# Kernel tuning notes

Measured on AMD Instinct MI355X. Metric: run time of the kernel, lower is better.

## Reference

```python
import jax, jax.numpy as jnp
import numpy as np

N_HEAD = 16

def _rope(t, cos, sin):
    # t: [B,T,H,hd]; cos/sin: [T, hd//2]
    B, T, H, hd = t.shape
    tr = t.reshape(B, T, H, hd // 2, 2)
    t0, t1 = tr[..., 0], tr[..., 1]
    c = cos[None, :T, None, :]
    s = sin[None, :T, None, :]
    out = jnp.stack([t0 * c - t1 * s, t0 * s + t1 * c], axis=-1)
    return out.reshape(B, T, H, hd)

def setup_inputs() -> dict:
    key = jax.random.key(0)
    B, T, D = 2, 2048, 1024
    hd = D // N_HEAD
    ks = jax.random.split(key, 5)
    x = jax.random.normal(ks[0], (B, T, D), dtype=jnp.float32)
    Wq = jax.random.normal(ks[1], (D, D), dtype=jnp.float32) * 0.02
    Wk = jax.random.normal(ks[2], (D, D), dtype=jnp.float32) * 0.02
    Wv = jax.random.normal(ks[3], (D, D), dtype=jnp.float32) * 0.02
    Wo = jax.random.normal(ks[4], (D, D), dtype=jnp.float32) * 0.02
    # Real rotary tables (cos/sin of theta-based angles), matching precompute_freqs_cis
    theta = 10000.0
    inv_freq = 1.0 / (theta ** (np.arange(0, hd, 2, dtype=np.float32) / hd))
    ang = np.outer(np.arange(T, dtype=np.float32), inv_freq)  # [T, hd//2]
    freqs_cos = jnp.asarray(np.cos(ang), dtype=jnp.float32)
    freqs_sin = jnp.asarray(np.sin(ang), dtype=jnp.float32)
    return {"x": x, "Wq": Wq, "Wk": Wk, "Wv": Wv, "Wo": Wo,
            "freqs_cos": freqs_cos, "freqs_sin": freqs_sin}

def reference(x, Wq, Wk, Wv, Wo, freqs_cos, freqs_sin):
    B, T, D = x.shape
    H = N_HEAD
    hd = D // H
    scale = hd ** -0.5
    q = (x @ Wq.T).reshape(B, T, H, hd)
    k = (x @ Wk.T).reshape(B, T, H, hd)
    v = (x @ Wv.T).reshape(B, T, H, hd)
    q = _rope(q, freqs_cos, freqs_sin)
    k = _rope(k, freqs_cos, freqs_sin)
    # scores: [B,H,T,T]
    scores = jnp.einsum('bqhd,bkhd->bhqk', q, k) * scale
    causal = jnp.tril(jnp.ones((T, T), dtype=bool))
    scores = jnp.where(causal[None, None], scores, -jnp.inf)
    attn = jax.nn.softmax(scores, axis=-1)
    out = jnp.einsum('bhqk,bkhd->bqhd', attn, v).reshape(B, T, D)
    return out @ Wo.T
```

## Files before the change

### kernel.cpp

```cpp
#include <hip/hip_runtime.h>
#include <math.h>

typedef __bf16 bf16;
typedef __bf16 bf16x8 __attribute__((ext_vector_type(8)));
typedef __bf16 bf16x4 __attribute__((ext_vector_type(4)));
typedef __bf16 bf16x2 __attribute__((ext_vector_type(2)));
typedef float  f32x4  __attribute__((ext_vector_type(4)));

#define B_DIM 2
#define T_LEN 2048
#define D_DIM 1024
#define N_HEAD 16
#define HEAD_D 64
#define M_ROWS (B_DIM * T_LEN)

#define GLDS16(g, l)                                                          \
    __builtin_amdgcn_global_load_lds(                                         \
        (const __attribute__((address_space(1))) void*)(g),                   \
        (__attribute__((address_space(3))) void*)(l), 16, 0, 0)

__global__ void prep_cvt(const float* __restrict__ x, const float* __restrict__ wq,
                         const float* __restrict__ wk, const float* __restrict__ wv,
                         const float* __restrict__ wo, bf16* __restrict__ xb,
                         bf16* __restrict__ wqkv, bf16* __restrict__ wob) {
    int id = blockIdx.x * blockDim.x + threadIdx.x;
    if (id >= (1 << 21)) return;
    const float* src; bf16* dst; int off;
    if (id < (1 << 20)) { src = x; dst = xb; off = id; }
    else {
        int r = id - (1 << 20);
        int wi = r >> 18;
        off = r & ((1 << 18) - 1);
        src = wi == 0 ? wq : wi == 1 ? wk : wi == 2 ? wv : wo;
        dst = wi < 3 ? wqkv + ((size_t)wi << 20) : wob;
    }
    float4 v = reinterpret_cast<const float4*>(src)[off];
    bf16x4 w;
    w[0] = (bf16)v.x; w[1] = (bf16)v.y; w[2] = (bf16)v.z; w[3] = (bf16)v.w;
    reinterpret_cast<bf16x4*>(dst)[off] = w;
}

template <int MODE>
__global__ __launch_bounds__(256, 4)
void gemm_glds(const bf16* __restrict__ A, const bf16* __restrict__ Bm,
               bf16* __restrict__ q, bf16* __restrict__ k, bf16* __restrict__ v,
               float* __restrict__ outf) {
    constexpr int K = D_DIM;
    __shared__ bf16 As[128 * 64];
    __shared__ bf16 Bs[128 * 64];
    const int tid = threadIdx.x, lane = tid & 63, wave = tid >> 6;
    const int wr = wave >> 1, wc = wave & 1;
    const int rowg = lane >> 4, col0 = lane & 15;

    const int nwg = gridDim.x * gridDim.y, cpx = nwg >> 3;
    const int lin = blockIdx.x + blockIdx.y * gridDim.x;
    const int nid = (lin & 7) * cpx + (lin >> 3);
    const int bx = nid % gridDim.x, by = nid / gridDim.x;
    const int m0 = by * 128, n0 = bx * 128;

    const int srow = lane >> 3;
    const int schk = (lane & 7) ^ srow;
    const bf16* gA = A + (size_t)(m0 + wave * 32 + srow) * K + schk * 8;
    const bf16* gB = Bm + (size_t)(n0 + wave * 32 + srow) * K + schk * 8;

    f32x4 acc[4][4];
    f32x4 zero = {0.f, 0.f, 0.f, 0.f};
#pragma unroll
    for (int i = 0; i < 4; i++)
#pragma unroll
        for (int j = 0; j < 4; j++) acc[i][j] = zero;

#pragma unroll 1
    for (int kt = 0; kt < 16; ++kt) {
        const int k0 = kt * 64;
#pragma unroll
        for (int t = 0; t < 4; ++t) {
            GLDS16(gA + k0 + t * 8 * K, &As[(wave * 32 + t * 8) * 64]);
            GLDS16(gB + k0 + t * 8 * K, &Bs[(wave * 32 + t * 8) * 64]);
        }
        __syncthreads();
#pragma unroll
        for (int kk = 0; kk < 2; ++kk) {
            bf16x8 af[4], bfr[4];
#pragma unroll
            for (int i = 0; i < 4; i++) {
                int R = wr * 64 + i * 16 + col0;
                af[i] = *reinterpret_cast<const bf16x8*>(&As[R * 64 + (((kk * 4 + rowg) ^ (R & 7)) * 8)]);
            }
#pragma unroll
            for (int j = 0; j < 4; j++) {
                int R = wc * 64 + j * 16 + col0;
                bfr[j] = *reinterpret_cast<const bf16x8*>(&Bs[R * 64 + (((kk * 4 + rowg) ^ (R & 7)) * 8)]);
            }
#pragma unroll
            for (int i = 0; i < 4; i++)
#pragma unroll
                for (int j = 0; j < 4; j++)
                    acc[i][j] = __builtin_amdgcn_mfma_f32_16x16x32_bf16(af[i], bfr[j], acc[i][j], 0, 0, 0);
        }
        __syncthreads();
    }

    if constexpr (MODE == 0) {
        const int which = bx >> 3;
        if (which < 2) {
            bf16* dst = which == 0 ? q : k;
#pragma unroll
            for (int i = 0; i < 4; i++)
#pragma unroll
                for (int j = 0; j < 4; j++)
#pragma unroll
                    for (int r = 0; r < 4; r++) {
                        int m = m0 + wr * 64 + i * 16 + rowg * 4 + r;
                        int n = (n0 + wc * 64 + j * 16 + col0) & 1023;
                        int b = m >> 11, t = m & 2047, h = n >> 6, d = n & 63;
                        dst[(((size_t)(b * N_HEAD + h)) * T_LEN + t) * HEAD_D + d] = (bf16)acc[i][j][r];
                    }
        } else {
#pragma unroll
            for (int i = 0; i < 4; i++)
#pragma unroll
                for (int j = 0; j < 4; j++) {
                    bf16x4 pk;
#pragma unroll
                    for (int r = 0; r < 4; r++) pk[r] = (bf16)acc[i][j][r];
                    int m = m0 + wr * 64 + i * 16 + rowg * 4;
                    int n = (n0 + wc * 64 + j * 16 + col0) & 1023;
                    int b = m >> 11, t = m & 2047, h = n >> 6, d = n & 63;
                    *reinterpret_cast<bf16x4*>(
                        &v[(((size_t)(b * N_HEAD + h)) * HEAD_D + d) * T_LEN + t]) = pk;
                }
        }
    } else {
#pragma unroll
        for (int i = 0; i < 4; i++)
#pragma unroll
            for (int j = 0; j < 4; j++)
#pragma unroll
                for (int r = 0; r < 4; r++) {
                    int m = m0 + wr * 64 + i * 16 + rowg * 4 + r;
                    int n = n0 + wc * 64 + j * 16 + col0;
                    outf[(size_t)m * D_DIM + n] = acc[i][j][r];
                }
    }
}

__global__ void rope_k(bf16* __restrict__ k, const float* __restrict__ cosT,
                       const float* __restrict__ sinT) {
    int id = blockIdx.x * blockDim.x + threadIdx.x;
    int i = id & 31;
    int t = (id >> 5) & 2047;
    int bh = id >> 16;
    float c = cosT[t * 32 + i], s = sinT[t * 32 + i];
    size_t p = ((size_t)bh * T_LEN + t) * HEAD_D + 2 * i;
    float k0 = (float)k[p], k1 = (float)k[p + 1];
    k[p]     = (bf16)(k0 * c - k1 * s);
    k[p + 1] = (bf16)(k0 * s + k1 * c);
}

__device__ inline bf16x8 rope8(bf16x8 v, f32x4 c4, f32x4 s4, float scale) {
    bf16x8 r;
#pragma unroll
    for (int m = 0; m < 4; ++m) {
        float a = (float)v[2 * m], b = (float)v[2 * m + 1];
        r[2 * m]     = (bf16)((a * c4[m] - b * s4[m]) * scale);
        r[2 * m + 1] = (bf16)((a * s4[m] + b * c4[m]) * scale);
    }
    return r;
}

__global__ __launch_bounds__(256, 3)
void attn_fwd(const bf16* __restrict__ qh, const bf16* __restrict__ kh,
              const bf16* __restrict__ vtg, const float* __restrict__ fc,
              const float* __restrict__ fs, bf16* __restrict__ ao) {
    __shared__ __align__(16) bf16 Ks[2][64 * 64];
    __shared__ __align__(16) bf16 Vs[2][64 * 64];
    __shared__ __align__(16) bf16 Ps[4][16][72];
    const int tid = threadIdx.x, lane = tid & 63, w = tid >> 6;
    const int g = lane >> 4, q15 = lane & 15;
    const int lin = blockIdx.x;
    const int xcd = lin & 7, idx = lin >> 3;
    const int qi = 31 - (idx >> 2);
    const int bh = xcd * 4 + (idx & 3);
    const size_t kbase = (size_t)bh * T_LEN * HEAD_D;
    const size_t vbase = (size_t)bh * HEAD_D * T_LEN;
    const int c0row = tid >> 3, ccg = tid & 7;
    const int swz = (ccg * 8) ^ ((c0row & 7) * 8);
    const int sel0 = c0row * 64 + swz;
    const int sel1 = sel0 + 32 * 64;
    const int ksw = (q15 & 7) * 8;

    const float NEGINF = -__builtin_inff();
    f32x4 zero = {0.f, 0.f, 0.f, 0.f};

    const int nt = qi + 1;
    const int qlo = qi * 64 + w * 16;

    bf16x8 aq[2];
#pragma unroll
    for (int kk = 0; kk < 2; ++kk) {
        bf16x8 qv = *reinterpret_cast<const bf16x8*>(
            &qh[kbase + (size_t)(qlo + q15) * HEAD_D + kk * 32 + g * 8]);
        f32x4 c4 = *reinterpret_cast<const f32x4*>(&fc[(qlo + q15) * 32 + kk * 16 + g * 4]);
        f32x4 s4 = *reinterpret_cast<const f32x4*>(&fs[(qlo + q15) * 32 + kk * 16 + g * 4]);
        aq[kk] = rope8(qv, c4, s4, 0.125f);
    }

    f32x4 o[4];
#pragma unroll
    for (int j = 0; j < 4; j++) o[j] = zero;
    float mi = NEGINF, li = 0.f;

    {
        uint4 k0a = *reinterpret_cast<const uint4*>(&kh[kbase + (size_t)c0row * HEAD_D + ccg * 8]);
        uint4 k0b = *reinterpret_cast<const uint4*>(&kh[kbase + (size_t)(c0row + 32) * HEAD_D + ccg * 8]);
        uint4 v0a = *reinterpret_cast<const uint4*>(&vtg[vbase + (size_t)c0row * T_LEN + ccg * 8]);
        uint4 v0b = *reinterpret_cast<const uint4*>(&vtg[vbase + (size_t)(c0row + 32) * T_LEN + ccg * 8]);
        *reinterpret_cast<uint4*>(&Ks[0][sel0]) = k0a;
        *reinterpret_cast<uint4*>(&Ks[0][sel1]) = k0b;
        *reinterpret_cast<uint4*>(&Vs[0][sel0]) = v0a;
        *reinterpret_cast<uint4*>(&Vs[0][sel1]) = v0b;
    }
    __syncthreads();

    for (int kt = 0; kt < nt; ++kt) {
        const int cur = kt & 1;
        const int kv0 = kt * 64;
        const bool pf = (kt + 1 < nt);
        uint4 kra, krb, vra, vrb;
        if (pf) {
            const int kn = kv0 + 64;
            kra = *reinterpret_cast<const uint4*>(&kh[kbase + (size_t)(kn + c0row) * HEAD_D + ccg * 8]);
            krb = *reinterpret_cast<const uint4*>(&kh[kbase + (size_t)(kn + c0row + 32) * HEAD_D + ccg * 8]);
            vra = *reinterpret_cast<const uint4*>(&vtg[vbase + (size_t)c0row * T_LEN + kn + ccg * 8]);
            vrb = *reinterpret_cast<const uint4*>(&vtg[vbase + (size_t)(c0row + 32) * T_LEN + kn + ccg * 8]);
        }

        f32x4 sT[4];
#pragma unroll
        for (int j = 0; j < 4; j++) sT[j] = zero;
        __builtin_amdgcn_s_setprio(1);
#pragma unroll
        for (int kk = 0; kk < 2; ++kk) {
            const int ko = (kk * 32 + g * 8) ^ ksw;
#pragma unroll
            for (int j = 0; j < 4; j++) {
                bf16x8 bk = *reinterpret_cast<const bf16x8*>(&Ks[cur][(j * 16 + q15) * 64 + ko]);
                sT[j] = __builtin_amdgcn_mfma_f32_16x16x32_bf16(bk, aq[kk], sT[j], 0, 0, 0);
            }
        }
        __builtin_amdgcn_s_setprio(0);
        if (kv0 + 63 > qlo) {
            const int qg = qlo + q15;
#pragma unroll
            for (int j = 0; j < 4; j++)
#pragma unroll
                for (int r = 0; r < 4; r++)
                    if (kv0 + j * 16 + g * 4 + r > qg) sT[j][r] = NEGINF;
        }
        float mx = sT[0][0];
#pragma unroll
        for (int j = 0; j < 4; j++)
#pragma unroll
            for (int r = 0; r < 4; r++) mx = fmaxf(mx, sT[j][r]);
        mx = fmaxf(mx, __shfl_xor(mx, 16));
        mx = fmaxf(mx, __shfl_xor(mx, 32));
        const float mnew = fmaxf(mi, mx);
        const float al = __expf(mi - mnew);
        float ps = 0.f;
#pragma unroll
        for (int j = 0; j < 4; j++)
#pragma unroll
            for (int r = 0; r < 4; r++) {
                float p = __expf(sT[j][r] - mnew);
                sT[j][r] = p;
                ps += p;
            }
        ps += __shfl_xor(ps, 16);
        ps += __shfl_xor(ps, 32);
        li = li * al + ps;
        mi = mnew;
#pragma unroll
        for (int j = 0; j < 4; j++)
#pragma unroll
            for (int pr = 0; pr < 2; ++pr) {
                bf16x2 pk;
                pk[0] = (bf16)sT[j][2 * pr];
                pk[1] = (bf16)sT[j][2 * pr + 1];
                *reinterpret_cast<bf16x2*>(&Ps[w][q15][j * 16 + g * 4 + 2 * pr]) = pk;
            }
#pragma unroll
        for (int j = 0; j < 4; j++)
#pragma unroll
            for (int r = 0; r < 4; r++) o[j][r] *= al;
        __builtin_amdgcn_s_setprio(1);
#pragma unroll
        for (int kk = 0; kk < 2; ++kk) {
            bf16x8 pb = *reinterpret_cast<const bf16x8*>(&Ps[w][q15][kk * 32 + g * 8]);
            const int ko = (kk * 32 + g * 8) ^ ksw;
#pragma unroll
            for (int j = 0; j < 4; j++) {
                bf16x8 av = *reinterpret_cast<const bf16x8*>(&Vs[cur][(j * 16 + q15) * 64 + ko]);
                o[j] = __builtin_amdgcn_mfma_f32_16x16x32_bf16(av, pb, o[j], 0, 0, 0);
            }
        }
        __builtin_amdgcn_s_setprio(0);
        if (pf) {
            *reinterpret_cast<uint4*>(&Ks[cur ^ 1][sel0]) = kra;
            *reinterpret_cast<uint4*>(&Ks[cur ^ 1][sel1]) = krb;
            *reinterpret_cast<uint4*>(&Vs[cur ^ 1][sel0]) = vra;
            *reinterpret_cast<uint4*>(&Vs[cur ^ 1][sel1]) = vrb;
        }
        __syncthreads();
    }

    const int b = bh >> 4, h = bh & 15;
    const float inv = 1.f / li;
    const int t = qlo + q15;
    bf16* dst = &ao[((size_t)(b * T_LEN + t)) * D_DIM + h * HEAD_D];
#pragma unroll
    for (int j = 0; j < 4; j++) {
        bf16x4 pk;
#pragma unroll
        for (int r = 0; r < 4; r++) pk[r] = (bf16)(o[j][r] * inv);
        *reinterpret_cast<bf16x4*>(&dst[j * 16 + g * 4]) = pk;
    }
}

extern "C" void kernel_launch(void* const* d_in, const int* in_sizes, int n_in,
                              void* d_out, int out_size, void* d_ws, size_t ws_size,
                              hipStream_t stream) {
    const float* x  = (const float*)d_in[0];
    const float* Wq = (const float*)d_in[1];
    const float* Wk = (const float*)d_in[2];
    const float* Wv = (const float*)d_in[3];
    const float* Wo = (const float*)d_in[4];
    const float* fc = (const float*)d_in[5];
    const float* fs = (const float*)d_in[6];
    float* out = (float*)d_out;

    char* ws = (char*)d_ws;
    const size_t MB = 1024 * 1024;
    bf16* xb   = (bf16*)(ws);
    bf16* wqkv = (bf16*)(ws + 8 * MB);
    bf16* wob  = (bf16*)(ws + 14 * MB);
    bf16* qhd  = (bf16*)(ws + 16 * MB);
    bf16* khd  = (bf16*)(ws + 24 * MB);
    bf16* vt   = (bf16*)(ws + 32 * MB);
    bf16* ao   = (bf16*)(ws + 40 * MB);

    prep_cvt<<<8192, 256, 0, stream>>>(x, Wq, Wk, Wv, Wo, xb, wqkv, wob);

    dim3 gq(24, 32);
    gemm_glds<0><<<gq, 256, 0, stream>>>(xb, wqkv, qhd, khd, vt, nullptr);

    rope_k<<<8192, 256, 0, stream>>>(khd, fc, fs);

    attn_fwd<<<1024, 256, 0, stream>>>(qhd, khd, vt, fc, fs, ao);

    dim3 go(8, 32);
    gemm_glds<1><<<go, 256, 0, stream>>>(ao, wob, nullptr, nullptr, nullptr, out);
}
```

Before: 107.2 us.

## Fuse RoPE into QKV GEMM epilogue and pass P through registers

Applies rotary embedding, plus a Q scale of 0.125·log2(e), inside the QKV projection epilogue using lane shuffles, which removes the separate K rope kernel and the in-attention Q rope. The attention softmax switches to exp2, skips rescaling the output accumulator unless the running max grows by more than a threshold, and moves the P operand between lanes with shuffles instead of an LDS round trip. Launch bounds rise to 4 waves per SIMD. The lazy rescale and the higher occupancy target trade some numerical headroom and register pressure for less work per tile.

```diff
diff --git a/kernel.cpp b/kernel.cpp
--- a/kernel.cpp
+++ b/kernel.cpp
@@ -13,11 +13,30 @@
 #define N_HEAD 16
 #define HEAD_D 64
 #define M_ROWS (B_DIM * T_LEN)
+#define QSCALE 0.18033688011112042f
 
 #define GLDS16(g, l)                                                          \
     __builtin_amdgcn_global_load_lds(                                         \
         (const __attribute__((address_space(1))) void*)(g),                   \
         (__attribute__((address_space(3))) void*)(l), 16, 0, 0)
+
+__device__ inline f32x4 vmax4(f32x4 a, f32x4 b) {
+    f32x4 r;
+#pragma unroll
+    for (int i = 0; i < 4; i++) r[i] = fmaxf(a[i], b[i]);
+    return r;
+}
+__device__ inline f32x4 vadd4(f32x4 a, f32x4 b) {
+    f32x4 r;
+#pragma unroll
+    for (int i = 0; i < 4; i++) r[i] = a[i] + b[i];
+    return r;
+}
+__device__ inline unsigned int pack2(float a, float b) {
+    bf16x2 t;
+    t[0] = (bf16)a; t[1] = (bf16)b;
+    return __builtin_bit_cast(unsigned int, t);
+}
 
 __global__ void prep_cvt(const float* __restrict__ x, const float* __restrict__ wq,
                          const float* __restrict__ wk, const float* __restrict__ wv,
@@ -44,7 +63,8 @@
 __global__ __launch_bounds__(256, 4)
 void gemm_glds(const bf16* __restrict__ A, const bf16* __restrict__ Bm,
                bf16* __restrict__ q, bf16* __restrict__ k, bf16* __restrict__ v,
-               float* __restrict__ outf) {
+               float* __restrict__ outf, const float* __restrict__ fc,
+               const float* __restrict__ fs) {
     constexpr int K = D_DIM;
     __shared__ bf16 As[128 * 64];
     __shared__ bf16 Bs[128 * 64];
@@ -105,17 +125,26 @@
         const int which = bx >> 3;
         if (which < 2) {
             bf16* dst = which == 0 ? q : k;
+            const float scale = which == 0 ? QSCALE : 1.0f;
+            const float sgnf = (col0 & 1) ? 1.f : -1.f;
 #pragma unroll
             for (int i = 0; i < 4; i++)
 #pragma unroll
-                for (int j = 0; j < 4; j++)
+                for (int j = 0; j < 4; j++) {
+                    int nn = (n0 + wc * 64 + j * 16 + col0) & 1023;
+                    int h = nn >> 6, d = nn & 63, i2 = d >> 1;
 #pragma unroll
                     for (int r = 0; r < 4; r++) {
                         int m = m0 + wr * 64 + i * 16 + rowg * 4 + r;
-                        int n = (n0 + wc * 64 + j * 16 + col0) & 1023;
-                        int b = m >> 11, t = m & 2047, h = n >> 6, d = n & 63;
-                        dst[(((size_t)(b * N_HEAD + h)) * T_LEN + t) * HEAD_D + d] = (bf16)acc[i][j][r];
+                        int b = m >> 11, t = m & 2047;
+                        float own = acc[i][j][r];
+                        float part = __shfl_xor(own, 1);
+                        float c = fc[t * 32 + i2], s = fs[t * 32 + i2];
+                        float res = own * c + part * (sgnf * s);
+                        dst[(((size_t)(b * N_HEAD + h)) * T_LEN + t) * HEAD_D + d] =
+                            (bf16)(res * scale);
                     }
+                }
         } else {
 #pragma unroll
             for (int i = 0; i < 4; i++)
@@ -145,37 +174,11 @@
     }
 }
 
-__global__ void rope_k(bf16* __restrict__ k, const float* __restrict__ cosT,
-                       const float* __restrict__ sinT) {
-    int id = blockIdx.x * blockDim.x + threadIdx.x;
-    int i = id & 31;
-    int t = (id >> 5) & 2047;
-    int bh = id >> 16;
-    float c = cosT[t * 32 + i], s = sinT[t * 32 + i];
-    size_t p = ((size_t)bh * T_LEN + t) * HEAD_D + 2 * i;
-    float k0 = (float)k[p], k1 = (float)k[p + 1];
-    k[p]     = (bf16)(k0 * c - k1 * s);
-    k[p + 1] = (bf16)(k0 * s + k1 * c);
-}
-
-__device__ inline bf16x8 rope8(bf16x8 v, f32x4 c4, f32x4 s4, float scale) {
-    bf16x8 r;
-#pragma unroll
-    for (int m = 0; m < 4; ++m) {
-        float a = (float)v[2 * m], b = (float)v[2 * m + 1];
-        r[2 * m]     = (bf16)((a * c4[m] - b * s4[m]) * scale);
-        r[2 * m + 1] = (bf16)((a * s4[m] + b * c4[m]) * scale);
-    }
-    return r;
-}
-
-__global__ __launch_bounds__(256, 3)
+__global__ __launch_bounds__(256, 4)
 void attn_fwd(const bf16* __restrict__ qh, const bf16* __restrict__ kh,
-              const bf16* __restrict__ vtg, const float* __restrict__ fc,
-              const float* __restrict__ fs, bf16* __restrict__ ao) {
+              const bf16* __restrict__ vtg, bf16* __restrict__ ao) {
     __shared__ __align__(16) bf16 Ks[2][64 * 64];
     __shared__ __align__(16) bf16 Vs[2][64 * 64];
-    __shared__ __align__(16) bf16 Ps[4][16][72];
     const int tid = threadIdx.x, lane = tid & 63, w = tid >> 6;
     const int g = lane >> 4, q15 = lane & 15;
     const int lin = blockIdx.x;
@@ -189,6 +192,9 @@
     const int sel0 = c0row * 64 + swz;
     const int sel1 = sel0 + 32 * 64;
     const int ksw = (q15 & 7) * 8;
+    const int sA = ((g & 1) << 5) | q15;
+    const int sB = sA | 16;
+    const bool hi = (g >= 2);
 
     const float NEGINF = -__builtin_inff();
     f32x4 zero = {0.f, 0.f, 0.f, 0.f};
@@ -198,13 +204,9 @@
 
     bf16x8 aq[2];
 #pragma unroll
-    for (int kk = 0; kk < 2; ++kk) {
-        bf16x8 qv = *reinterpret_cast<const bf16x8*>(
+    for (int kk = 0; kk < 2; ++kk)
+        aq[kk] = *reinterpret_cast<const bf16x8*>(
             &qh[kbase + (size_t)(qlo + q15) * HEAD_D + kk * 32 + g * 8]);
-        f32x4 c4 = *reinterpret_cast<const f32x4*>(&fc[(qlo + q15) * 32 + kk * 16 + g * 4]);
-        f32x4 s4 = *reinterpret_cast<const f32x4*>(&fs[(qlo + q15) * 32 + kk * 16 + g * 4]);
-        aq[kk] = rope8(qv, c4, s4, 0.125f);
-    }
 
     f32x4 o[4];
 #pragma unroll
@@ -258,45 +260,49 @@
                 for (int r = 0; r < 4; r++)
                     if (kv0 + j * 16 + g * 4 + r > qg) sT[j][r] = NEGINF;
         }
-        float mx = sT[0][0];
-#pragma unroll
-        for (int j = 0; j < 4; j++)
-#pragma unroll
-            for (int r = 0; r < 4; r++) mx = fmaxf(mx, sT[j][r]);
+        f32x4 t0 = vmax4(sT[0], sT[1]), t1 = vmax4(sT[2], sT[3]);
+        t0 = vmax4(t0, t1);
+        float mx = fmaxf(fmaxf(t0[0], t0[1]), fmaxf(t0[2], t0[3]));
         mx = fmaxf(mx, __shfl_xor(mx, 16));
         mx = fmaxf(mx, __shfl_xor(mx, 32));
-        const float mnew = fmaxf(mi, mx);
-        const float al = __expf(mi - mnew);
-        float ps = 0.f;
+        if (!__all(mx <= mi + 8.f)) {
+            const float mnew = fmaxf(mi, mx);
+            const float al = __builtin_exp2f(mi - mnew);
+#pragma unroll
+            for (int j = 0; j < 4; j++)
+#pragma unroll
+                for (int r = 0; r < 4; r++) o[j][r] *= al;
+            li *= al;
+            mi = mnew;
+        }
 #pragma unroll
         for (int j = 0; j < 4; j++)
 #pragma unroll
-            for (int r = 0; r < 4; r++) {
-                float p = __expf(sT[j][r] - mnew);
-                sT[j][r] = p;
-                ps += p;
-            }
+            for (int r = 0; r < 4; r++) sT[j][r] = __builtin_exp2f(sT[j][r] - mi);
+        f32x4 a0 = vadd4(sT[0], sT[1]), a1 = vadd4(sT[2], sT[3]);
+        a0 = vadd4(a0, a1);
+        float ps = (a0[0] + a0[1]) + (a0[2] + a0[3]);
         ps += __shfl_xor(ps, 16);
         ps += __shfl_xor(ps, 32);
-        li = li * al + ps;
-        mi = mnew;
-#pragma unroll
-        for (int j = 0; j < 4; j++)
-#pragma unroll
-            for (int pr = 0; pr < 2; ++pr) {
-                bf16x2 pk;
-                pk[0] = (bf16)sT[j][2 * pr];
-                pk[1] = (bf16)sT[j][2 * pr + 1];
-                *reinterpret_cast<bf16x2*>(&Ps[w][q15][j * 16 + g * 4 + 2 * pr]) = pk;
-            }
-#pragma unroll
-        for (int j = 0; j < 4; j++)
-#pragma unroll
-            for (int r = 0; r < 4; r++) o[j][r] *= al;
+        li += ps;
+
+        unsigned int pw[8];
+#pragma unroll
+        for (int j = 0; j < 4; j++) {
+            pw[2 * j]     = pack2(sT[j][0], sT[j][1]);
+            pw[2 * j + 1] = pack2(sT[j][2], sT[j][3]);
+        }
         __builtin_amdgcn_s_setprio(1);
 #pragma unroll
         for (int kk = 0; kk < 2; ++kk) {
-            bf16x8 pb = *reinterpret_cast<const bf16x8*>(&Ps[w][q15][kk * 32 + g * 8]);
+            unsigned int c00 = __shfl(pw[kk * 4 + 0], sA), c01 = __shfl(pw[kk * 4 + 1], sA);
+            unsigned int c20 = __shfl(pw[kk * 4 + 2], sA), c21 = __shfl(pw[kk * 4 + 3], sA);
+            unsigned int d00 = __shfl(pw[kk * 4 + 0], sB), d01 = __shfl(pw[kk * 4 + 1], sB);
+            unsigned int d20 = __shfl(pw[kk * 4 + 2], sB), d21 = __shfl(pw[kk * 4 + 3], sB);
+            uint4 pkd;
+            pkd.x = hi ? c20 : c00; pkd.y = hi ? c21 : c01;
+            pkd.z = hi ? d20 : d00; pkd.w = hi ? d21 : d01;
+            bf16x8 pb = __builtin_bit_cast(bf16x8, pkd);
             const int ko = (kk * 32 + g * 8) ^ ksw;
 #pragma unroll
             for (int j = 0; j < 4; j++) {
@@ -352,12 +358,10 @@
     prep_cvt<<<8192, 256, 0, stream>>>(x, Wq, Wk, Wv, Wo, xb, wqkv, wob);
 
     dim3 gq(24, 32);
-    gemm_glds<0><<<gq, 256, 0, stream>>>(xb, wqkv, qhd, khd, vt, nullptr);
-
-    rope_k<<<8192, 256, 0, stream>>>(khd, fc, fs);
-
-    attn_fwd<<<1024, 256, 0, stream>>>(qhd, khd, vt, fc, fs, ao);
+    gemm_glds<0><<<gq, 256, 0, stream>>>(xb, wqkv, qhd, khd, vt, nullptr, fc, fs);
+
+    attn_fwd<<<1024, 256, 0, stream>>>(qhd, khd, vt, ao);
 
     dim3 go(8, 32);
-    gemm_glds<1><<<go, 256, 0, stream>>>(ao, wob, nullptr, nullptr, nullptr, out);
-}
+    gemm_glds<1><<<go, 256, 0, stream>>>(ao, wob, nullptr, nullptr, nullptr, out, fc, fs);
+}
```

Result: slower. 115.2 us (+7.5%).
